# Performance work log

Hardware: AMD Instinct MI355X
Metric: run time of the kernel (lower is better)

## Reference

```python
import jax, jax.numpy as jnp
import numpy as np

MLP_CHANNELS = 128
MLP_KERNEL = 5


def setup_inputs() -> dict:
    key = jax.random.key(0)
    k1, k2 = jax.random.split(key)
    b, c, h, w = 16, MLP_CHANNELS, 128, 128
    num_w = MLP_KERNEL ** 2 * c + c  # 3328
    inp = jax.random.normal(k1, (b, c, h, w), dtype=jnp.float32)
    # mimic ini_weights_ scaling: conv weights ~ N(0, 6/(k^2+c)), bias ~ N(0, 1/c)
    weights = jax.random.normal(k2, (b, num_w), dtype=jnp.float32)
    off = MLP_KERNEL ** 2 * c
    scale = jnp.concatenate([
        jnp.full((off,), np.sqrt(6.0 / (MLP_KERNEL ** 2 + c)), dtype=jnp.float32),
        jnp.full((c,), np.sqrt(1.0 / c), dtype=jnp.float32),
    ])
    weights = weights * scale[None, :]
    return {"input": inp, "weights": weights}


def reference(input, weights):
    b, c, h, w = input.shape
    k = MLP_KERNEL
    off = k * k * c
    # per-sample depthwise filters [b, c, 1, k, k] and biases [b, c]
    wk = weights[:, :off].reshape(b, c, 1, k, k)
    bias = weights[:, off:off + c]

    def dwconv(x, wt):
        # x: [c,h,w], wt: [c,1,k,k]; depthwise conv via feature_group_count=c
        return jax.lax.conv_general_dilated(
            x[None], wt, window_strides=(1, 1), padding='SAME',
            dimension_numbers=('NCHW', 'OIHW', 'NCHW'),
            feature_group_count=c)[0]

    out = jax.vmap(dwconv)(input, wk)          # [b,c,h,w]
    out = out + bias[:, :, None, None]          # fused bias
    return jax.nn.silu(out)                     # act
```

## Files before the change

### kernel.cpp

```cpp
#include <hip/hip_runtime.h>
#include <math.h>

#define C_CH 128
#define HW 128
#define KK 5
#define PAD 2
#define TILE_ROWS 32
#define LDS_ROWS (TILE_ROWS + 2*PAD)
#define NW (KK*KK*C_CH + C_CH)
#define N_TILES (HW / TILE_ROWS)
#define CHUNKS ((LDS_ROWS * HW * 4) / 1024)

__global__ __launch_bounds__(256, 8) void hyperconv_dw_silu(
    const float* __restrict__ inp, const float* __restrict__ wts,
    float* __restrict__ out)
{
    __shared__ float s[LDS_ROWS][HW];

    const int tid  = threadIdx.x;
    const int tile = blockIdx.x;
    const int c    = blockIdx.y;
    const int b    = blockIdx.z;

    const float* wt = wts + (size_t)b * NW;
    float wk[25];
#pragma unroll
    for (int j = 0; j < 25; ++j) wk[j] = wt[c * 25 + j];
    const float bias = wt[KK * KK * C_CH + c];

    const int row0 = tile * TILE_ROWS;
    const float* plane = inp + ((size_t)(b * C_CH + c)) * (HW * HW);
    const float* src0  = plane + (row0 - PAD) * HW;

    const int wave = tid >> 6;
    const int lane = tid & 63;

    for (int ch = wave; ch < CHUNKS; ch += 4) {
        const bool oob = (tile == 0 && ch == 0) ||
                         (tile == N_TILES - 1 && ch == CHUNKS - 1);
        if (!oob) {
            __builtin_amdgcn_global_load_lds(
                (const __attribute__((address_space(1))) void*)(src0 + ch * 256 + lane * 4),
                (__attribute__((address_space(3))) void*)((char*)&s[0][0] + ch * 1024),
                16, 0, 0);
        }
    }
    if (tile == 0 && tid < 64)
        *(float4*)((char*)&s[0][0] + tid * 16) = make_float4(0.f, 0.f, 0.f, 0.f);
    if (tile == N_TILES - 1 && tid < 64)
        *(float4*)((char*)&s[0][0] + (CHUNKS - 1) * 1024 + tid * 16) =
            make_float4(0.f, 0.f, 0.f, 0.f);
    __syncthreads();

    const int colg = tid & 31;
    const int rowg = tid >> 5;
    const int ro   = rowg * 4;
    const int xb   = colg * 4;

    const int lcb = (colg == 0)  ? 0   : (xb - 4);
    const int rcb = (colg == 31) ? 120 : (xb + 4);

    float acc[4][4];
#pragma unroll
    for (int i = 0; i < 4; ++i)
#pragma unroll
        for (int j = 0; j < 4; ++j) acc[i][j] = bias;

#pragma unroll
    for (int r = 0; r < 8; ++r) {
        const float* srow = &s[ro + r][0];
        const float4 xl = *(const float4*)(srow + lcb);
        const float4 xm = *(const float4*)(srow + xb);
        const float4 xr = *(const float4*)(srow + rcb);
        float x[8];
        x[0] = (colg == 0)  ? 0.f : xl.z;
        x[1] = (colg == 0)  ? 0.f : xl.w;
        x[2] = xm.x; x[3] = xm.y; x[4] = xm.z; x[5] = xm.w;
        x[6] = (colg == 31) ? 0.f : xr.x;
        x[7] = (colg == 31) ? 0.f : xr.y;

#pragma unroll
        for (int orow = 0; orow < 4; ++orow) {
            const int kh = r - orow;
            if (kh < 0 || kh > 4) continue;
#pragma unroll
            for (int oc = 0; oc < 4; ++oc)
#pragma unroll
                for (int kw = 0; kw < 5; ++kw)
                    acc[orow][oc] = fmaf(wk[kh * 5 + kw], x[oc + kw], acc[orow][oc]);
        }
    }

    float* oplane = out + ((size_t)(b * C_CH + c)) * (HW * HW);
#pragma unroll
    for (int orow = 0; orow < 4; ++orow) {
        float v0 = acc[orow][0], v1 = acc[orow][1];
        float v2 = acc[orow][2], v3 = acc[orow][3];
        float4 o;
        o.x = v0 * __builtin_amdgcn_rcpf(1.0f + __expf(-v0));
        o.y = v1 * __builtin_amdgcn_rcpf(1.0f + __expf(-v1));
        o.z = v2 * __builtin_amdgcn_rcpf(1.0f + __expf(-v2));
        o.w = v3 * __builtin_amdgcn_rcpf(1.0f + __expf(-v3));
        *(float4*)(oplane + (size_t)(row0 + ro + orow) * HW + xb) = o;
    }
}

extern "C" void kernel_launch(void* const* d_in, const int* in_sizes, int n_in,
                              void* d_out, int out_size, void* d_ws, size_t ws_size,
                              hipStream_t stream) {
    const float* inp = (const float*)d_in[0];
    const float* wts = (const float*)d_in[1];
    float* out = (float*)d_out;

    const int batch = in_sizes[1] / NW;
    dim3 grid(N_TILES, C_CH, batch);
    hyperconv_dw_silu<<<grid, 256, 0, stream>>>(inp, wts, out);
}
```

Measured before the change: 243.3 us.

## Process whole plane per block with double-buffered async LDS staging

Each block now covers an entire channel plane, with four 32-row tiles in sequence, instead of one tile. Two LDS buffers are filled with global_load_lds, and hand-tuned vmcnt waits let the next tile's load overlap the current tile's compute. This also avoids refetching halo rows and reloading weights for every tile. In exchange there are four times fewer blocks, occupancy drops to 4 blocks per SIMD because LDS use doubles, and correctness depends on fragile hand-counted waitcnt values.

Result: faster. 233.4 us (-4.1%).

```diff
diff --git a/kernel.cpp b/kernel.cpp
--- a/kernel.cpp
+++ b/kernel.cpp
@@ -4,59 +4,48 @@
 #define C_CH 128
 #define HW 128
 #define KK 5
-#define PAD 2
-#define TILE_ROWS 32
-#define LDS_ROWS (TILE_ROWS + 2*PAD)
 #define NW (KK*KK*C_CH + C_CH)
-#define N_TILES (HW / TILE_ROWS)
-#define CHUNKS ((LDS_ROWS * HW * 4) / 1024)
+#define TROWS 32
+#define LROWS 36
+#define WSPAN 4608
 
-__global__ __launch_bounds__(256, 8) void hyperconv_dw_silu(
-    const float* __restrict__ inp, const float* __restrict__ wts,
-    float* __restrict__ out)
-{
-    __shared__ float s[LDS_ROWS][HW];
+typedef const __attribute__((address_space(1))) void* gp_t;
+typedef __attribute__((address_space(3))) void* lp_t;
 
-    const int tid  = threadIdx.x;
-    const int tile = blockIdx.x;
-    const int c    = blockIdx.y;
-    const int b    = blockIdx.z;
+__device__ __forceinline__ void ld16(const char* g, char* l, int lane) {
+    __builtin_amdgcn_global_load_lds((gp_t)(g + lane * 16), (lp_t)l, 16, 0, 0);
+}
+__device__ __forceinline__ void ld4(const char* g, char* l, int lane) {
+    __builtin_amdgcn_global_load_lds((gp_t)(g + lane * 4), (lp_t)l, 4, 0, 0);
+}
 
-    const float* wt = wts + (size_t)b * NW;
-    float wk[25];
-#pragma unroll
-    for (int j = 0; j < 25; ++j) wk[j] = wt[c * 25 + j];
-    const float bias = wt[KK * KK * C_CH + c];
+__device__ __forceinline__ void stage(const float* plane, int t, float* buf,
+                                      int wave, int lane, int skipmode) {
+    const char* g = (const char*)plane + (long)(TROWS * t - 2) * (HW * 4) + wave * WSPAN;
+    char* l = (char*)buf + wave * WSPAN;
+    if (wave < 3) {
+        if (!(skipmode == 1 && wave == 0)) ld16(g, l, lane);
+        ld16(g + 1024, l + 1024, lane);
+        ld16(g + 2048, l + 2048, lane);
+        ld16(g + 3072, l + 3072, lane);
+        ld4 (g + 4096, l + 4096, lane);
+        ld4 (g + 4352, l + 4352, lane);
+    } else {
+        ld4 (g,        l,        lane);
+        ld4 (g + 256,  l + 256,  lane);
+        ld16(g + 512,  l + 512,  lane);
+        ld16(g + 1536, l + 1536, lane);
+        ld16(g + 2560, l + 2560, lane);
+        if (skipmode != 2) ld16(g + 3584, l + 3584, lane);
+    }
+}
 
-    const int row0 = tile * TILE_ROWS;
-    const float* plane = inp + ((size_t)(b * C_CH + c)) * (HW * HW);
-    const float* src0  = plane + (row0 - PAD) * HW;
-
-    const int wave = tid >> 6;
-    const int lane = tid & 63;
-
-    for (int ch = wave; ch < CHUNKS; ch += 4) {
-        const bool oob = (tile == 0 && ch == 0) ||
-                         (tile == N_TILES - 1 && ch == CHUNKS - 1);
-        if (!oob) {
-            __builtin_amdgcn_global_load_lds(
-                (const __attribute__((address_space(1))) void*)(src0 + ch * 256 + lane * 4),
-                (__attribute__((address_space(3))) void*)((char*)&s[0][0] + ch * 1024),
-                16, 0, 0);
-        }
-    }
-    if (tile == 0 && tid < 64)
-        *(float4*)((char*)&s[0][0] + tid * 16) = make_float4(0.f, 0.f, 0.f, 0.f);
-    if (tile == N_TILES - 1 && tid < 64)
-        *(float4*)((char*)&s[0][0] + (CHUNKS - 1) * 1024 + tid * 16) =
-            make_float4(0.f, 0.f, 0.f, 0.f);
-    __syncthreads();
-
-    const int colg = tid & 31;
-    const int rowg = tid >> 5;
-    const int ro   = rowg * 4;
-    const int xb   = colg * 4;
-
+__device__ __forceinline__ void compute_tile(const float (*s)[HW], int t,
+                                             int rowg, int colg,
+                                             const float* wk, float bias,
+                                             float* oplane) {
+    const int ro = rowg * 4;
+    const int xb = colg * 4;
     const int lcb = (colg == 0)  ? 0   : (xb - 4);
     const int rcb = (colg == 31) ? 120 : (xb + 4);
 
@@ -91,7 +80,6 @@
         }
     }
 
-    float* oplane = out + ((size_t)(b * C_CH + c)) * (HW * HW);
 #pragma unroll
     for (int orow = 0; orow < 4; ++orow) {
         float v0 = acc[orow][0], v1 = acc[orow][1];
@@ -101,8 +89,64 @@
         o.y = v1 * __builtin_amdgcn_rcpf(1.0f + __expf(-v1));
         o.z = v2 * __builtin_amdgcn_rcpf(1.0f + __expf(-v2));
         o.w = v3 * __builtin_amdgcn_rcpf(1.0f + __expf(-v3));
-        *(float4*)(oplane + (size_t)(row0 + ro + orow) * HW + xb) = o;
+        *(float4*)(oplane + (size_t)(TROWS * t + ro + orow) * HW + xb) = o;
     }
+}
+
+#define PHASE_SYNC(str) do { \
+    asm volatile(str ::: "memory"); \
+    __builtin_amdgcn_sched_barrier(0); \
+    __builtin_amdgcn_s_barrier(); \
+    __builtin_amdgcn_sched_barrier(0); } while (0)
+
+__global__ __launch_bounds__(256, 4) void hyperconv_dw_silu(
+    const float* __restrict__ inp, const float* __restrict__ wts,
+    float* __restrict__ out)
+{
+    __shared__ float sA[LROWS][HW];
+    __shared__ float sB[LROWS][HW];
+
+    const int tid  = threadIdx.x;
+    const int wave = tid >> 6;
+    const int lane = tid & 63;
+    const int c    = blockIdx.x;
+    const int b    = blockIdx.y;
+
+    const float* wt = wts + (size_t)b * NW;
+    float wk[25];
+#pragma unroll
+    for (int j = 0; j < 25; ++j) wk[j] = wt[c * 25 + j];
+    const float bias = wt[KK * KK * C_CH + c];
+
+    const float* plane  = inp + ((size_t)(b * C_CH + c)) * (HW * HW);
+    float*       oplane = out + ((size_t)(b * C_CH + c)) * (HW * HW);
+
+    const int colg = tid & 31;
+    const int rowg = tid >> 5;
+
+    stage(plane, 0, &sA[0][0], wave, lane, 1);
+    if (tid < 64)
+        *(float4*)((char*)&sA[0][0] + tid * 16) = make_float4(0.f, 0.f, 0.f, 0.f);
+    stage(plane, 1, &sB[0][0], wave, lane, 0);
+
+    PHASE_SYNC("s_waitcnt vmcnt(6) lgkmcnt(0)");
+    compute_tile(sA, 0, rowg, colg, wk, bias, oplane);
+    PHASE_SYNC("s_waitcnt lgkmcnt(0)");
+    stage(plane, 2, &sA[0][0], wave, lane, 0);
+
+    PHASE_SYNC("s_waitcnt vmcnt(10)");
+    compute_tile(sB, 1, rowg, colg, wk, bias, oplane);
+    PHASE_SYNC("s_waitcnt lgkmcnt(0)");
+    stage(plane, 3, &sB[0][0], wave, lane, 2);
+    if (wave == 3)
+        *(float4*)((char*)&sB[0][0] + 17408 + lane * 16) =
+            make_float4(0.f, 0.f, 0.f, 0.f);
+
+    PHASE_SYNC("s_waitcnt vmcnt(9)");
+    compute_tile(sA, 2, rowg, colg, wk, bias, oplane);
+
+    PHASE_SYNC("s_waitcnt vmcnt(4) lgkmcnt(0)");
+    compute_tile(sB, 3, rowg, colg, wk, bias, oplane);
 }
 
 extern "C" void kernel_launch(void* const* d_in, const int* in_sizes, int n_in,
@@ -113,6 +157,6 @@
     float* out = (float*)d_out;
 
     const int batch = in_sizes[1] / NW;
-    dim3 grid(N_TILES, C_CH, batch);
+    dim3 grid(C_CH, batch);
     hyperconv_dw_silu<<<grid, 256, 0, stream>>>(inp, wts, out);
 }
```

## Replace LDS tiling with register sliding-window over rows loaded directly from global

Applied to the files above, without the earlier changes.

Removes the shared-memory staging and barrier. Each block now processes a whole channel plane, with each thread sweeping 16 rows and holding a 5-row sliding window of inputs in registers, loaded straight from global memory with clamped rows and zero masking. This is meant to avoid the LDS round trip and the halo re-reads between tiles, and it cuts the grid to one block per (channel, batch). In exchange it depends on L1/L2 to serve the overlapping row and column reads, has fewer blocks, and lowers the launch-bounds occupancy hint to 6.

New measurement: 246.2 us. No clear change (+1.2%).

```diff
diff --git a/kernel.cpp b/kernel.cpp
--- a/kernel.cpp
+++ b/kernel.cpp
@@ -4,23 +4,16 @@
 #define C_CH 128
 #define HW 128
 #define KK 5
-#define PAD 2
-#define TILE_ROWS 32
-#define LDS_ROWS (TILE_ROWS + 2*PAD)
 #define NW (KK*KK*C_CH + C_CH)
-#define N_TILES (HW / TILE_ROWS)
-#define CHUNKS ((LDS_ROWS * HW * 4) / 1024)
+#define RPT 16
 
-__global__ __launch_bounds__(256, 8) void hyperconv_dw_silu(
+__global__ __launch_bounds__(256, 6) void hyperconv_dw_silu(
     const float* __restrict__ inp, const float* __restrict__ wts,
     float* __restrict__ out)
 {
-    __shared__ float s[LDS_ROWS][HW];
-
-    const int tid  = threadIdx.x;
-    const int tile = blockIdx.x;
-    const int c    = blockIdx.y;
-    const int b    = blockIdx.z;
+    const int tid = threadIdx.x;
+    const int c   = blockIdx.x;
+    const int b   = blockIdx.y;
 
     const float* wt = wts + (size_t)b * NW;
     float wk[25];
@@ -28,80 +21,61 @@
     for (int j = 0; j < 25; ++j) wk[j] = wt[c * 25 + j];
     const float bias = wt[KK * KK * C_CH + c];
 
-    const int row0 = tile * TILE_ROWS;
-    const float* plane = inp + ((size_t)(b * C_CH + c)) * (HW * HW);
-    const float* src0  = plane + (row0 - PAD) * HW;
-
-    const int wave = tid >> 6;
-    const int lane = tid & 63;
-
-    for (int ch = wave; ch < CHUNKS; ch += 4) {
-        const bool oob = (tile == 0 && ch == 0) ||
-                         (tile == N_TILES - 1 && ch == CHUNKS - 1);
-        if (!oob) {
-            __builtin_amdgcn_global_load_lds(
-                (const __attribute__((address_space(1))) void*)(src0 + ch * 256 + lane * 4),
-                (__attribute__((address_space(3))) void*)((char*)&s[0][0] + ch * 1024),
-                16, 0, 0);
-        }
-    }
-    if (tile == 0 && tid < 64)
-        *(float4*)((char*)&s[0][0] + tid * 16) = make_float4(0.f, 0.f, 0.f, 0.f);
-    if (tile == N_TILES - 1 && tid < 64)
-        *(float4*)((char*)&s[0][0] + (CHUNKS - 1) * 1024 + tid * 16) =
-            make_float4(0.f, 0.f, 0.f, 0.f);
-    __syncthreads();
+    const float* plane  = inp + ((size_t)(b * C_CH + c)) * (HW * HW);
+    float*       oplane = out + ((size_t)(b * C_CH + c)) * (HW * HW);
 
     const int colg = tid & 31;
     const int rowg = tid >> 5;
-    const int ro   = rowg * 4;
+    const int r0   = rowg * RPT;
     const int xb   = colg * 4;
+    const int lcb  = (colg == 0)  ? 0   : (xb - 4);
+    const int rcb  = (colg == 31) ? 120 : (xb + 4);
 
-    const int lcb = (colg == 0)  ? 0   : (xb - 4);
-    const int rcb = (colg == 31) ? 120 : (xb + 4);
+    float w[5][8];
 
-    float acc[4][4];
-#pragma unroll
-    for (int i = 0; i < 4; ++i)
-#pragma unroll
-        for (int j = 0; j < 4; ++j) acc[i][j] = bias;
+    auto load_row = [&](int ir, float* wr) {
+        const int irc = (ir < 0) ? 0 : ((ir > 127) ? 127 : ir);
+        const float* row = plane + irc * HW;
+        const float4 xl = *(const float4*)(row + lcb);
+        const float4 xm = *(const float4*)(row + xb);
+        const float4 xr = *(const float4*)(row + rcb);
+        const bool vz = (ir < 0) | (ir > 127);
+        const bool lz = vz | (colg == 0);
+        const bool rz = vz | (colg == 31);
+        wr[0] = lz ? 0.f : xl.z;
+        wr[1] = lz ? 0.f : xl.w;
+        wr[2] = vz ? 0.f : xm.x;
+        wr[3] = vz ? 0.f : xm.y;
+        wr[4] = vz ? 0.f : xm.z;
+        wr[5] = vz ? 0.f : xm.w;
+        wr[6] = rz ? 0.f : xr.x;
+        wr[7] = rz ? 0.f : xr.y;
+    };
 
 #pragma unroll
-    for (int r = 0; r < 8; ++r) {
-        const float* srow = &s[ro + r][0];
-        const float4 xl = *(const float4*)(srow + lcb);
-        const float4 xm = *(const float4*)(srow + xb);
-        const float4 xr = *(const float4*)(srow + rcb);
-        float x[8];
-        x[0] = (colg == 0)  ? 0.f : xl.z;
-        x[1] = (colg == 0)  ? 0.f : xl.w;
-        x[2] = xm.x; x[3] = xm.y; x[4] = xm.z; x[5] = xm.w;
-        x[6] = (colg == 31) ? 0.f : xr.x;
-        x[7] = (colg == 31) ? 0.f : xr.y;
+    for (int i = 0; i < 4; ++i) load_row(r0 - 2 + i, w[i]);
 
 #pragma unroll
-        for (int orow = 0; orow < 4; ++orow) {
-            const int kh = r - orow;
-            if (kh < 0 || kh > 4) continue;
+    for (int s = 0; s < RPT; ++s) {
+        load_row(r0 + s + 2, w[(s + 4) % 5]);
+
+        float acc[4] = {bias, bias, bias, bias};
+#pragma unroll
+        for (int kh = 0; kh < 5; ++kh) {
+            const float* wr = w[(s + kh) % 5];
 #pragma unroll
             for (int oc = 0; oc < 4; ++oc)
 #pragma unroll
                 for (int kw = 0; kw < 5; ++kw)
-                    acc[orow][oc] = fmaf(wk[kh * 5 + kw], x[oc + kw], acc[orow][oc]);
+                    acc[oc] = fmaf(wk[kh * 5 + kw], wr[oc + kw], acc[oc]);
         }
-    }
 
-    float* oplane = out + ((size_t)(b * C_CH + c)) * (HW * HW);
-#pragma unroll
-    for (int orow = 0; orow < 4; ++orow) {
-        float v0 = acc[orow][0], v1 = acc[orow][1];
-        float v2 = acc[orow][2], v3 = acc[orow][3];
         float4 o;
-        o.x = v0 * __builtin_amdgcn_rcpf(1.0f + __expf(-v0));
-        o.y = v1 * __builtin_amdgcn_rcpf(1.0f + __expf(-v1));
-        o.z = v2 * __builtin_amdgcn_rcpf(1.0f + __expf(-v2));
-        o.w = v3 * __builtin_amdgcn_rcpf(1.0f + __expf(-v3));
-        *(float4*)(oplane + (size_t)(row0 + ro + orow) * HW + xb) = o;
+        o.x = acc[0] * __builtin_amdgcn_rcpf(1.0f + __expf(-acc[0]));
+        o.y = acc[1] * __builtin_amdgcn_rcpf(1.0f + __expf(-acc[1]));
+        o.z = acc[2] * __builtin_amdgcn_rcpf(1.0f + __expf(-acc[2]));
+        o.w = acc[3] * __builtin_amdgcn_rcpf(1.0f + __expf(-acc[3]));
+        *(float4*)(oplane + (size_t)(r0 + s) * HW + xb) = o;
     }
 }
 
@@ -113,6 +87,6 @@
     float* out = (float*)d_out;
 
     const int batch = in_sizes[1] / NW;
-    dim3 grid(N_TILES, C_CH, batch);
+    dim3 grid(C_CH, batch);
     hyperconv_dw_silu<<<grid, 256, 0, stream>>>(inp, wts, out);
 }
```
